# Kernel optimization log

Hardware: AMD Instinct MI355X
Metric: run time of the kernel (lower is better)

Reference implementation:

```python
import jax, jax.numpy as jnp
import numpy as np

GAMMA = 0.98
STEP_TYPE_LAST = 2  # ALF StepType.LAST
T, B = 256, 65536


def setup_inputs() -> dict:
    key = jax.random.key(0)
    ks = jax.random.split(key, 6)
    reward = jax.random.normal(ks[0], (T, B), jnp.float32)
    discount = jnp.ones((T, B), jnp.float32)
    value = jax.random.normal(ks[1], (T, B), jnp.float32)
    target_value = jax.random.normal(ks[2], (T, B), jnp.float32)
    b = jax.random.randint(ks[3], (T, B), 0, 2).astype(jnp.int32)
    rollout_b = jax.random.randint(ks[4], (T, B), 0, 2).astype(jnp.int32)
    step_type = jax.random.randint(ks[5], (T, B), 0, 3).astype(jnp.int32)
    return {"reward": reward, "discount": discount, "value": value,
            "target_value": target_value, "b": b, "rollout_b": rollout_b,
            "step_type": step_type}


def reference(reward, discount, value, target_value, b, rollout_b, step_type):
    discounts = discount * GAMMA                      # [T,B]
    bb = rollout_b.astype(bool) | b.astype(bool)      # compare-through beta actions
    bb = bb.at[0].set(False)
    is_lasts = ((step_type == STEP_TYPE_LAST) | bb).astype(jnp.float32)  # [T,B]

    # _discounted_return: backward recursion over time (T > 2 path)
    #   rets[t] = acc[t+1] * discounts[t+1] + rewards[t+1]
    #   acc[t]  = is_lasts[t] * values[t] + (1 - is_lasts[t]) * rets[t]
    def step(acc_next, xs):
        disc_n, rew_n, val_t, il_t = xs
        ret_t = acc_next * disc_n + rew_n
        acc_t = il_t * val_t + (1.0 - il_t) * ret_t
        return acc_t, ret_t

    xs = (discounts[1:], reward[1:], target_value[:-1], is_lasts[:-1])
    _, rets = jax.lax.scan(step, target_value[-1], xs, reverse=True)  # [T-1,B]

    returns = jax.lax.stop_gradient(rets)             # detached target
    loss = jnp.square(returns - value[:-1])           # element-wise squared TD loss
    # tensor_extend_zero: pad a zero row at the end -> [T,B]
    return jnp.concatenate([loss, jnp.zeros_like(loss[:1])], axis=0)
```

## Files before the change

### kernel.cpp

```cpp
#include <hip/hip_runtime.h>


#define GAMMA_F 0.98f

constexpr int T = 256;
constexpr int B = 65536;

__global__ __launch_bounds__(256) void td_loss_kernel(
    const float* __restrict__ reward,
    const float* __restrict__ discount,
    const float* __restrict__ value,
    const float* __restrict__ target_value,
    const int*   __restrict__ b_arr,
    const int*   __restrict__ rollout_b,
    const int*   __restrict__ step_type,
    float*       __restrict__ out)
{
    const int col = blockIdx.x * blockDim.x + threadIdx.x;
    if (col >= B) return;

    float acc = target_value[(size_t)(T - 1) * B + col];
    out[(size_t)(T - 1) * B + col] = 0.0f;

    #pragma unroll 4
    for (int t = T - 2; t >= 0; --t) {
        const size_t idx_t = (size_t)t * B + col;
        const size_t idx_n = idx_t + B;

        const float disc_n = discount[idx_n] * GAMMA_F;
        const float rew_n  = reward[idx_n];
        const float val_t  = target_value[idx_t];
        const float v_t    = value[idx_t];
        const int   st     = step_type[idx_t];
        const int   bbv    = (t > 0) ? (rollout_b[idx_t] | b_arr[idx_t]) : 0;

        const float il  = ((st == 2) || (bbv != 0)) ? 1.0f : 0.0f;
        const float ret = acc * disc_n + rew_n;
        acc = il * val_t + (1.0f - il) * ret;

        const float d = ret - v_t;
        out[idx_t] = d * d;
    }
}

extern "C" void kernel_launch(void* const* d_in, const int* in_sizes, int n_in,
                              void* d_out, int out_size, void* d_ws, size_t ws_size,
                              hipStream_t stream) {
    const float* reward       = (const float*)d_in[0];
    const float* discount     = (const float*)d_in[1];
    const float* value        = (const float*)d_in[2];
    const float* target_value = (const float*)d_in[3];
    const int*   b_arr        = (const int*)d_in[4];
    const int*   rollout_b    = (const int*)d_in[5];
    const int*   step_type    = (const int*)d_in[6];
    float*       out          = (float*)d_out;

    const int threads = 256;
    const int blocks  = B / threads;
    td_loss_kernel<<<blocks, threads, 0, stream>>>(
        reward, discount, value, target_value, b_arr, rollout_b, step_type, out);
}
```

Before: 446.1 us.

## Vectorize columns as float2 and software-pipeline time-step loads with register ring

Each thread now handles two adjacent columns through float2/int2 loads. A register ring holds the inputs for the next five time steps, so loads for future steps are in flight while the serial recurrence runs. Blocks shrink to 64 threads with half as many total threads. This is meant to hide the DRAM latency of the serial backward scan, at the cost of more registers and fewer waves for latency hiding.

```diff
diff --git a/kernel.cpp b/kernel.cpp
--- a/kernel.cpp
+++ b/kernel.cpp
@@ -5,8 +5,11 @@
 
 constexpr int T = 256;
 constexpr int B = 65536;
+constexpr int S = B / 2;
+constexpr int NSTEP = T - 1;
+constexpr int D = 5;
 
-__global__ __launch_bounds__(256) void td_loss_kernel(
+__global__ __launch_bounds__(64, 1) void td_loss_kernel(
     const float* __restrict__ reward,
     const float* __restrict__ discount,
     const float* __restrict__ value,
@@ -16,30 +19,68 @@
     const int*   __restrict__ step_type,
     float*       __restrict__ out)
 {
-    const int col = blockIdx.x * blockDim.x + threadIdx.x;
-    if (col >= B) return;
+    const int lane = blockIdx.x * 64 + threadIdx.x;
 
-    float acc = target_value[(size_t)(T - 1) * B + col];
-    out[(size_t)(T - 1) * B + col] = 0.0f;
+    const float2* rw2 = (const float2*)reward;
+    const float2* dc2 = (const float2*)discount;
+    const float2* vl2 = (const float2*)value;
+    const float2* tv2 = (const float2*)target_value;
+    const int2*   b2  = (const int2*)b_arr;
+    const int2*   rb2 = (const int2*)rollout_b;
+    const int2*   st2 = (const int2*)step_type;
+    float2*       ot2 = (float2*)out;
 
-    #pragma unroll 4
-    for (int t = T - 2; t >= 0; --t) {
-        const size_t idx_t = (size_t)t * B + col;
-        const size_t idx_n = idx_t + B;
+    float2 pd[D], pr[D], pv[D], pt[D];
+    int2   pb[D], prb[D], pst[D];
 
-        const float disc_n = discount[idx_n] * GAMMA_F;
-        const float rew_n  = reward[idx_n];
-        const float val_t  = target_value[idx_t];
-        const float v_t    = value[idx_t];
-        const int   st     = step_type[idx_t];
-        const int   bbv    = (t > 0) ? (rollout_b[idx_t] | b_arr[idx_t]) : 0;
+    float2 acc = tv2[(size_t)(T - 1) * S + lane];
+    ot2[(size_t)(T - 1) * S + lane] = make_float2(0.0f, 0.0f);
 
-        const float il  = ((st == 2) || (bbv != 0)) ? 1.0f : 0.0f;
-        const float ret = acc * disc_n + rew_n;
-        acc = il * val_t + (1.0f - il) * ret;
+    #pragma unroll
+    for (int j = 0; j < D; ++j) {
+        const int t = NSTEP - 1 - j;
+        const size_t it = (size_t)t * S + lane;
+        pd[j]  = dc2[it + S];
+        pr[j]  = rw2[it + S];
+        pv[j]  = vl2[it];
+        pt[j]  = tv2[it];
+        pb[j]  = b2[it];
+        prb[j] = rb2[it];
+        pst[j] = st2[it];
+    }
 
-        const float d = ret - v_t;
-        out[idx_t] = d * d;
+    #pragma unroll 1
+    for (int s0 = 0; s0 < NSTEP; s0 += D) {
+        #pragma unroll
+        for (int j = 0; j < D; ++j) {
+            const int s = s0 + j;
+            const int t = NSTEP - 1 - s;
+
+            const float dx = pd[j].x * GAMMA_F;
+            const float dy = pd[j].y * GAMMA_F;
+            const float retx = acc.x * dx + pr[j].x;
+            const float rety = acc.y * dy + pr[j].y;
+            const bool ilx = (pst[j].x == 2) || ((t > 0) && ((pb[j].x | prb[j].x) != 0));
+            const bool ily = (pst[j].y == 2) || ((t > 0) && ((pb[j].y | prb[j].y) != 0));
+            acc.x = ilx ? pt[j].x : retx;
+            acc.y = ily ? pt[j].y : rety;
+            const float ddx = retx - pv[j].x;
+            const float ddy = rety - pv[j].y;
+            ot2[(size_t)t * S + lane] = make_float2(ddx * ddx, ddy * ddy);
+
+            const int sp = s + D;
+            if (sp < NSTEP) {
+                const int tp = NSTEP - 1 - sp;
+                const size_t it = (size_t)tp * S + lane;
+                pd[j]  = dc2[it + S];
+                pr[j]  = rw2[it + S];
+                pv[j]  = vl2[it];
+                pt[j]  = tv2[it];
+                pb[j]  = b2[it];
+                prb[j] = rb2[it];
+                pst[j] = st2[it];
+            }
+        }
     }
 }
 
@@ -55,8 +96,8 @@
     const int*   step_type    = (const int*)d_in[6];
     float*       out          = (float*)d_out;
 
-    const int threads = 256;
-    const int blocks  = B / threads;
+    const int threads = 64;
+    const int blocks  = (B / 2) / threads;
     td_loss_kernel<<<blocks, threads, 0, stream>>>(
         reward, discount, value, target_value, b_arr, rollout_b, step_type, out);
 }
```

New measurement: 413.8 us. 7.2% less time.

## Software-pipeline the backward scan with depth-5 register prefetch and float2 columns

Applied to the files above, without the earlier changes.

Each thread now handles two adjacent columns through 8-byte vector loads and stores. A 5-deep register ring buffer prefetches the seven input streams several timesteps ahead, with sched_barrier used to pin the ordering. Blocks shrink to one wave of 64 threads, giving 512 blocks in total. The aim is to hide per-step global-load latency in the serial time recursion, which is bandwidth and latency bound. In exchange it uses many more registers and launches far fewer threads, which may leave too few waves in flight to saturate HBM.

```diff
diff --git a/kernel.cpp b/kernel.cpp
--- a/kernel.cpp
+++ b/kernel.cpp
@@ -5,8 +5,44 @@
 
 constexpr int T = 256;
 constexpr int B = 65536;
+constexpr int S = B / 2;
+constexpr int D = 5;
 
-__global__ __launch_bounds__(256) void td_loss_kernel(
+typedef float f32x2 __attribute__((ext_vector_type(2)));
+typedef int   i32x2 __attribute__((ext_vector_type(2)));
+
+#define SB() __builtin_amdgcn_sched_barrier(0)
+
+#define PREFETCH(j, t) do {                  \
+    const size_t it_ = (size_t)(t) * S + lane; \
+    pd[j]  = dc2[it_ + S];                   \
+    pr[j]  = rw2[it_ + S];                   \
+    pv[j]  = vl2[it_];                       \
+    pt[j]  = tv2[it_];                       \
+    pb[j]  = b2[it_];                        \
+    prb[j] = rb2[it_];                       \
+    pst[j] = st2[it_];                       \
+} while (0)
+
+#define CONSUME(j, t, T0) do {                                      \
+    const float retx_ = acc.x * (pd[j].x * GAMMA_F) + pr[j].x;      \
+    const float rety_ = acc.y * (pd[j].y * GAMMA_F) + pr[j].y;      \
+    const bool ilx_ = (pst[j].x == 2) || ((T0) && ((pb[j].x | prb[j].x) != 0)); \
+    const bool ily_ = (pst[j].y == 2) || ((T0) && ((pb[j].y | prb[j].y) != 0)); \
+    acc.x = ilx_ ? pt[j].x : retx_;                                 \
+    acc.y = ily_ ? pt[j].y : rety_;                                 \
+    f32x2 o_;                                                       \
+    o_.x = (retx_ - pv[j].x) * (retx_ - pv[j].x);                   \
+    o_.y = (rety_ - pv[j].y) * (rety_ - pv[j].y);                   \
+    ot2[(size_t)(t) * S + lane] = o_;                               \
+} while (0)
+
+#define STEP(j, t) do {                      \
+    SB(); CONSUME(j, (t), true);             \
+    SB(); PREFETCH(j, (t) - D);              \
+} while (0)
+
+__global__ __launch_bounds__(64, 1) void td_loss_kernel(
     const float* __restrict__ reward,
     const float* __restrict__ discount,
     const float* __restrict__ value,
@@ -16,31 +52,44 @@
     const int*   __restrict__ step_type,
     float*       __restrict__ out)
 {
-    const int col = blockIdx.x * blockDim.x + threadIdx.x;
-    if (col >= B) return;
+    const int lane = blockIdx.x * 64 + threadIdx.x;
 
-    float acc = target_value[(size_t)(T - 1) * B + col];
-    out[(size_t)(T - 1) * B + col] = 0.0f;
+    const f32x2* rw2 = (const f32x2*)reward;
+    const f32x2* dc2 = (const f32x2*)discount;
+    const f32x2* vl2 = (const f32x2*)value;
+    const f32x2* tv2 = (const f32x2*)target_value;
+    const i32x2* b2  = (const i32x2*)b_arr;
+    const i32x2* rb2 = (const i32x2*)rollout_b;
+    const i32x2* st2 = (const i32x2*)step_type;
+    f32x2*       ot2 = (f32x2*)out;
 
-    #pragma unroll 4
-    for (int t = T - 2; t >= 0; --t) {
-        const size_t idx_t = (size_t)t * B + col;
-        const size_t idx_n = idx_t + B;
+    f32x2 pd[D], pr[D], pv[D], pt[D];
+    i32x2 pb[D], prb[D], pst[D];
 
-        const float disc_n = discount[idx_n] * GAMMA_F;
-        const float rew_n  = reward[idx_n];
-        const float val_t  = target_value[idx_t];
-        const float v_t    = value[idx_t];
-        const int   st     = step_type[idx_t];
-        const int   bbv    = (t > 0) ? (rollout_b[idx_t] | b_arr[idx_t]) : 0;
+    f32x2 acc = tv2[(size_t)(T - 1) * S + lane];
 
-        const float il  = ((st == 2) || (bbv != 0)) ? 1.0f : 0.0f;
-        const float ret = acc * disc_n + rew_n;
-        acc = il * val_t + (1.0f - il) * ret;
+    f32x2 z_; z_.x = 0.0f; z_.y = 0.0f;
+    ot2[(size_t)(T - 1) * S + lane] = z_;
 
-        const float d = ret - v_t;
-        out[idx_t] = d * d;
+    SB();
+    PREFETCH(0, 254); PREFETCH(1, 253); PREFETCH(2, 252);
+    PREFETCH(3, 251); PREFETCH(4, 250);
+
+    #pragma unroll 1
+    for (int s0 = 0; s0 < 250; s0 += 5) {
+        const int t0 = 254 - s0;
+        STEP(0, t0);
+        STEP(1, t0 - 1);
+        STEP(2, t0 - 2);
+        STEP(3, t0 - 3);
+        STEP(4, t0 - 4);
     }
+
+    SB(); CONSUME(0, 4, true);
+    SB(); CONSUME(1, 3, true);
+    SB(); CONSUME(2, 2, true);
+    SB(); CONSUME(3, 1, true);
+    SB(); CONSUME(4, 0, false);
 }
 
 extern "C" void kernel_launch(void* const* d_in, const int* in_sizes, int n_in,
@@ -55,8 +104,8 @@
     const int*   step_type    = (const int*)d_in[6];
     float*       out          = (float*)d_out;
 
-    const int threads = 256;
-    const int blocks  = B / threads;
+    const int threads = 64;
+    const int blocks  = (B / 2) / threads;
     td_loss_kernel<<<blocks, threads, 0, stream>>>(
         reward, discount, value, target_value, b_arr, rollout_b, step_type, out);
 }
```

Measured after the change: 406.1 us. -9.0%, faster.

## Split time axis into chunks seeded by scanning forward to the next reset

Applied to the files above, without the earlier changes.

The backward scan over T is cut into 8 time chunks processed by separate blocks, and each thread handles two columns with 2-wide vector loads. A non-final chunk first scans forward from its boundary to the nearest is_last step, where the accumulator resets to target_value, then runs the recurrence backward from there to rebuild its starting state. The aim is more parallelism (more blocks and loads in flight) than one thread per column walking all 256 steps. In exchange it adds redundant reads during the seeding pass. That pass is cheap only because resets occur with high probability in the test data; with rare resets it would reread long stretches of the input.

```diff
diff --git a/kernel.cpp b/kernel.cpp
--- a/kernel.cpp
+++ b/kernel.cpp
@@ -5,6 +5,13 @@
 
 constexpr int T = 256;
 constexpr int B = 65536;
+constexpr int S = B / 2;
+constexpr int C = 8;
+constexpr int L = T / C;
+constexpr int COLB = S / 256;
+
+typedef float f32x2 __attribute__((ext_vector_type(2)));
+typedef int   i32x2 __attribute__((ext_vector_type(2)));
 
 __global__ __launch_bounds__(256) void td_loss_kernel(
     const float* __restrict__ reward,
@@ -16,30 +23,87 @@
     const int*   __restrict__ step_type,
     float*       __restrict__ out)
 {
-    const int col = blockIdx.x * blockDim.x + threadIdx.x;
-    if (col >= B) return;
+    const int lane = (blockIdx.x & (COLB - 1)) * 256 + threadIdx.x;
+    const int c    = blockIdx.x >> 7;
 
-    float acc = target_value[(size_t)(T - 1) * B + col];
-    out[(size_t)(T - 1) * B + col] = 0.0f;
+    const f32x2* rw2 = (const f32x2*)reward;
+    const f32x2* dc2 = (const f32x2*)discount;
+    const f32x2* vl2 = (const f32x2*)value;
+    const f32x2* tv2 = (const f32x2*)target_value;
+    const i32x2* b2  = (const i32x2*)b_arr;
+    const i32x2* rb2 = (const i32x2*)rollout_b;
+    const i32x2* st2 = (const i32x2*)step_type;
+    f32x2*       ot2 = (f32x2*)out;
 
-    #pragma unroll 4
-    for (int t = T - 2; t >= 0; --t) {
-        const size_t idx_t = (size_t)t * B + col;
-        const size_t idx_n = idx_t + B;
+    f32x2 acc;
+    int tend;
 
-        const float disc_n = discount[idx_n] * GAMMA_F;
-        const float rew_n  = reward[idx_n];
-        const float val_t  = target_value[idx_t];
-        const float v_t    = value[idx_t];
-        const int   st     = step_type[idx_t];
-        const int   bbv    = (t > 0) ? (rollout_b[idx_t] | b_arr[idx_t]) : 0;
+    if (c == C - 1) {
+        acc = tv2[(size_t)(T - 1) * S + lane];
+        f32x2 z; z.x = 0.0f; z.y = 0.0f;
+        ot2[(size_t)(T - 1) * S + lane] = z;
+        tend = T - 2;
+    } else {
+        const int p = (c + 1) * L;
 
-        const float il  = ((st == 2) || (bbv != 0)) ? 1.0f : 0.0f;
-        const float ret = acc * disc_n + rew_n;
-        acc = il * val_t + (1.0f - il) * ret;
+        int  tsx = T - 1, tsy = T - 1;
+        bool rx = false, ry = false;
+        for (int t = p; t <= T - 2; ++t) {
+            const size_t it = (size_t)t * S + lane;
+            const i32x2 st = st2[it];
+            const i32x2 bb = b2[it];
+            const i32x2 rb = rb2[it];
+            const bool ilx = (st.x == 2) || ((bb.x | rb.x) != 0);
+            const bool ily = (st.y == 2) || ((bb.y | rb.y) != 0);
+            if (ilx && !rx) { tsx = t; rx = true; }
+            if (ily && !ry) { tsy = t; ry = true; }
+            if (__all(rx && ry)) break;
+        }
 
-        const float d = ret - v_t;
-        out[idx_t] = d * d;
+        float ax = target_value[(size_t)tsx * B + 2 * lane];
+        float ay = target_value[(size_t)tsy * B + 2 * lane + 1];
+
+        int tm = (tsx > tsy) ? tsx : tsy;
+        #pragma unroll
+        for (int off = 32; off > 0; off >>= 1) {
+            const int o = __shfl_xor(tm, off);
+            tm = (o > tm) ? o : tm;
+        }
+        for (int t = tm - 1; t >= p; --t) {
+            const size_t in = (size_t)(t + 1) * S + lane;
+            const f32x2 dn = dc2[in];
+            const f32x2 rn = rw2[in];
+            if (t < tsx) ax = ax * (dn.x * GAMMA_F) + rn.x;
+            if (t < tsy) ay = ay * (dn.y * GAMMA_F) + rn.y;
+        }
+        acc.x = ax; acc.y = ay;
+        tend = p - 1;
+    }
+
+    const int tlo = c * L;
+    for (int t = tend; t >= tlo; --t) {
+        const size_t it = (size_t)t * S + lane;
+        const size_t in = it + S;
+        const f32x2 dn = dc2[in];
+        const f32x2 rn = rw2[in];
+        const f32x2 vv = vl2[it];
+        const f32x2 tv = tv2[it];
+        const i32x2 st = st2[it];
+        const i32x2 bb = b2[it];
+        const i32x2 rb = rb2[it];
+
+        const float retx = acc.x * (dn.x * GAMMA_F) + rn.x;
+        const float rety = acc.y * (dn.y * GAMMA_F) + rn.y;
+        const bool t0  = (t > 0);
+        const bool ilx = (st.x == 2) || (t0 && ((bb.x | rb.x) != 0));
+        const bool ily = (st.y == 2) || (t0 && ((bb.y | rb.y) != 0));
+        acc.x = ilx ? tv.x : retx;
+        acc.y = ily ? tv.y : rety;
+
+        f32x2 o;
+        o.x = (retx - vv.x) * (retx - vv.x);
+        o.y = (rety - vv.y) * (rety - vv.y);
+        ot2[it] = o;
     }
 }
 
@@ -55,8 +119,7 @@
     const int*   step_type    = (const int*)d_in[6];
     float*       out          = (float*)d_out;
 
-    const int threads = 256;
-    const int blocks  = B / threads;
-    td_loss_kernel<<<blocks, threads, 0, stream>>>(
+    const int blocks = C * COLB;
+    td_loss_kernel<<<blocks, 256, 0, stream>>>(
         reward, discount, value, target_value, b_arr, rollout_b, step_type, out);
 }
```

Measured after the change: 424.8 us. 1.05x faster.
